# Optimization experiments

Measured on AMD Instinct MI355X. Metric: run time of the kernel, lower is better.

Reference implementation:

```python
import jax, jax.numpy as jnp
import numpy as np

AVG_NOBJ = 49.0
NEG_SLOPE = 0.01  # torch leaky_relu default


def eops_1_to_2(x, nobj, aggregation):
    """x: [B,N,C] -> [B,C,5,N,N] equivariant basis (rank-1 -> rank-2)."""
    B, N, C = x.shape
    xt = jnp.transpose(x, (0, 2, 1))  # B,C,N
    if aggregation == 'sum':
        agg = xt.sum(-1) / AVG_NOBJ                      # B,C
    elif aggregation == 'mean':
        agg = xt.sum(-1) / nobj[:, None]                 # B,C
    elif aggregation == 'max':
        agg = xt.max(-1)
    elif aggregation == 'min':
        agg = xt.min(-1)
    eye = jnp.eye(N, dtype=x.dtype)                      # N,N
    op1 = xt[:, :, :, None] * eye                        # x_i on diagonal
    op2 = jnp.broadcast_to(xt[:, :, None, :], (B, C, N, N))  # x_j along rows
    op3 = jnp.broadcast_to(xt[:, :, :, None], (B, C, N, N))  # x_i along cols
    op4 = agg[:, :, None, None] * eye                    # agg on diagonal
    op5 = jnp.broadcast_to(agg[:, :, None, None], (B, C, N, N))  # agg everywhere
    return jnp.stack([op1, op2, op3, op4, op5], axis=2)  # B,C,5,N,N


def setup_inputs() -> dict:
    key = jax.random.key(0)
    k1, k2 = jax.random.split(key)
    B, N, C, S = 8, 128, 64, 64
    basis_total = 5 * 4  # 5 basis ops per config char, config='smxn'
    inputs = jax.random.normal(k1, (B, N, C), dtype=jnp.float32)
    mask = jnp.ones((B, N, N, 1), dtype=jnp.float32)
    nobj = jnp.full((B,), 100.0, dtype=jnp.float32)
    coefs = jax.random.normal(k2, (C, S, basis_total), dtype=jnp.float32) * np.sqrt(2.0 / (C * basis_total)).astype(np.float32)
    bias = jnp.zeros((S,), dtype=jnp.float32)
    return {"inputs": inputs, "mask": mask, "nobj": nobj, "coefs": coefs, "bias": bias}


def reference(inputs, mask, nobj, coefs, bias):
    # config = 'smxn' -> sum, mean, max, min basis tensors, concat on basis axis
    ops = jnp.concatenate(
        [eops_1_to_2(inputs, nobj, a) for a in ('sum', 'mean', 'max', 'min')],
        axis=2)  # B,C,20,N,N
    out = jnp.einsum('dsb,ndbij->nijs', coefs, ops)      # B,N,N,S
    out = out + bias[None, None, None, :]
    out = jnp.where(out >= 0, out, NEG_SLOPE * out)      # leaky_relu
    return out * mask
```

## Files before the change

kernel.cpp:

```cpp
#include <hip/hip_runtime.h>

constexpr int B = 8, N = 128, C = 64, S = 64;
constexpr float INV_AVG = 1.0f / 49.0f;
constexpr float SLOPE = 0.01f;

typedef float f4 __attribute__((ext_vector_type(4)));

constexpr int WS_A  = 0;
constexpr int WS_R  = 65536;
constexpr int WS_C  = 131072;
constexpr int WS_D  = 196608;
constexpr int WS_E  = 197120;

__global__ __launch_bounds__(256) void prep_kernel(
    const float* __restrict__ x,
    const float* __restrict__ nobj,
    const float* __restrict__ coefs,
    float* __restrict__ ws)
{
  __shared__ float smem[13312];
  const int tid = threadIdx.x;

  if (blockIdx.x < 64) {
    float* W1 = smem;
    float* W2 = smem + 4096;
    float* W3 = smem + 8192;
    float* xs = smem + 12288;
    const int n  = blockIdx.x >> 3;
    const int i0 = (blockIdx.x & 7) << 4;

#pragma unroll
    for (int k = 0; k < 16; ++k) {
      const int e = k * 256 + tid;
      const float4* cp = (const float4*)(coefs + e * 20);
      float4 f0 = cp[0], f1 = cp[1], f2 = cp[2], f3 = cp[3], f4v = cp[4];
      W1[e] = f0.x + f1.y + f2.z + f3.w;
      W2[e] = f0.y + f1.z + f2.w + f4v.x;
      W3[e] = f0.z + f1.w + f3.x + f4v.y;
    }
    ((float4*)xs)[tid] = ((const float4*)(x + (n * N + i0) * C))[tid];
    __syncthreads();

    const int s = tid & 63;
    const int g = tid >> 6;
    float a1[4] = {0,0,0,0}, a2[4] = {0,0,0,0}, a3[4] = {0,0,0,0};
#pragma unroll 8
    for (int d = 0; d < 64; ++d) {
      float w1 = W1[d * 64 + s];
      float w2 = W2[d * 64 + s];
      float w3 = W3[d * 64 + s];
#pragma unroll
      for (int k = 0; k < 4; ++k) {
        float xv = xs[(g * 4 + k) * 64 + d];
        a1[k] += xv * w1;
        a2[k] += xv * w2;
        a3[k] += xv * w3;
      }
    }
#pragma unroll
    for (int k = 0; k < 4; ++k) {
      const int o = (n * N + i0 + g * 4 + k) * S + s;
      ws[WS_A + o] = a1[k];
      ws[WS_R + o] = a2[k];
      ws[WS_C + o] = a3[k];
    }
  } else {
    const int n = blockIdx.x - 64;
    float* xs  = smem;
    float* ps  = smem + 8192;
    float* pmx = smem + 8448;
    float* pmn = smem + 8704;
    float* ag  = smem + 8960;

    const float4* xg = (const float4*)(x + n * N * C);
    float4* xs4 = (float4*)xs;
#pragma unroll
    for (int k = 0; k < 8; ++k) xs4[tid + k * 256] = xg[tid + k * 256];
    __syncthreads();

    const int d = tid & 63, grp = tid >> 6;
    float sm = 0.f, mx = -INFINITY, mn = INFINITY;
    for (int i = grp * 32; i < grp * 32 + 32; ++i) {
      float v = xs[i * 64 + d];
      sm += v;
      mx = fmaxf(mx, v);
      mn = fminf(mn, v);
    }
    ps [grp * 64 + d] = sm;
    pmx[grp * 64 + d] = mx;
    pmn[grp * 64 + d] = mn;
    __syncthreads();

    if (tid < 64) {
      float s0 = ps[tid] + ps[64 + tid] + ps[128 + tid] + ps[192 + tid];
      float m0 = fmaxf(fmaxf(pmx[tid], pmx[64 + tid]),
                       fmaxf(pmx[128 + tid], pmx[192 + tid]));
      float n0 = fminf(fminf(pmn[tid], pmn[64 + tid]),
                       fminf(pmn[128 + tid], pmn[192 + tid]));
      ag[tid]       = s0 * INV_AVG;
      ag[64 + tid]  = s0 / nobj[n];
      ag[128 + tid] = m0;
      ag[192 + tid] = n0;
    }
    __syncthreads();

    if (tid < 64) {
      const int s = tid;
      float dv = 0.f, ev = 0.f;
      for (int d2 = 0; d2 < 64; ++d2) {
        const float* cp = coefs + d2 * (S * 20) + s * 20;
        float a0 = ag[d2], a1 = ag[64 + d2], a2 = ag[128 + d2], a3 = ag[192 + d2];
        dv += a0 * cp[3] + a1 * cp[8] + a2 * cp[13] + a3 * cp[18];
        ev += a0 * cp[4] + a1 * cp[9] + a2 * cp[14] + a3 * cp[19];
      }
      ws[WS_D + n * S + s] = dv;
      ws[WS_E + n * S + s] = ev;
    }
  }
}

__global__ __launch_bounds__(256) void assemble_kernel(
    const float* __restrict__ ws,
    const float* __restrict__ mask,
    const float* __restrict__ bias,
    float* __restrict__ out)
{
  const int bi = blockIdx.x;
  const int n  = bi >> 7;
  const int i  = bi & 127;
  const int l  = threadIdx.x & 15;
  const int jg = threadIdx.x >> 4;

  const float4* A4 = (const float4*)(ws + WS_A);
  const float4* R4 = (const float4*)(ws + WS_R);
  const float4* C4 = (const float4*)(ws + WS_C);
  const float4* D4 = (const float4*)(ws + WS_D);
  const float4* E4 = (const float4*)(ws + WS_E);

  float4 cc = C4[bi * 16 + l];
  float4 ee = E4[n * 16 + l];
  float4 bb = ((const float4*)bias)[l];
  float bx = cc.x + ee.x + bb.x;
  float by = cc.y + ee.y + bb.y;
  float bz = cc.z + ee.z + bb.z;
  float bw = cc.w + ee.w + bb.w;

  f4* out4 = (f4*)out + (size_t)bi * (N * 16);

#pragma unroll
  for (int t = 0; t < 8; ++t) {
    const int j = jg + t * 16;
    float4 rr = R4[(n * N + j) * 16 + l];
    float  m  = mask[bi * N + j];
    float v0 = bx + rr.x;
    float v1 = by + rr.y;
    float v2 = bz + rr.z;
    float v3 = bw + rr.w;
    if (j == i) {
      float4 aa = A4[bi * 16 + l];
      float4 dd = D4[n * 16 + l];
      v0 += aa.x + dd.x; v1 += aa.y + dd.y;
      v2 += aa.z + dd.z; v3 += aa.w + dd.w;
    }
    v0 = (v0 >= 0.f) ? v0 : SLOPE * v0;
    v1 = (v1 >= 0.f) ? v1 : SLOPE * v1;
    v2 = (v2 >= 0.f) ? v2 : SLOPE * v2;
    v3 = (v3 >= 0.f) ? v3 : SLOPE * v3;
    f4 o;
    o.x = v0 * m; o.y = v1 * m; o.z = v2 * m; o.w = v3 * m;
    __builtin_nontemporal_store(o, &out4[j * 16 + l]);
  }
}

extern "C" void kernel_launch(void* const* d_in, const int* in_sizes, int n_in,
                              void* d_out, int out_size, void* d_ws, size_t ws_size,
                              hipStream_t stream) {
  const float* x     = (const float*)d_in[0];
  const float* mask  = (const float*)d_in[1];
  const float* nobj  = (const float*)d_in[2];
  const float* coefs = (const float*)d_in[3];
  const float* bias  = (const float*)d_in[4];
  float* out = (float*)d_out;
  float* ws  = (float*)d_ws;

  prep_kernel<<<72, 256, 0, stream>>>(x, nobj, coefs, ws);
  assemble_kernel<<<1024, 256, 0, stream>>>(ws, mask, bias, out);
}
```

Baseline: 83.13 us.

## Fuse prep and assemble kernels into a single kernel with redundant per-block recompute

Merges the two-kernel pipeline into one kernel of 256 blocks. Each block handles 4 rows i and recomputes the per-batch aggregates, the combined coefficient matrices, the row term for all 128 j, and the D/E terms from shared memory, then writes the output directly. This removes the second launch and the workspace round trip through global memory. In exchange, every block redoes the 64x64 coefficient reduction and the R projection for its batch (32x redundant work), and there are fewer blocks to hide the store-bound output write.

```diff
diff --git a/kernel.cpp b/kernel.cpp
--- a/kernel.cpp
+++ b/kernel.cpp
@@ -1,174 +1,163 @@
 #include <hip/hip_runtime.h>
 
-constexpr int B = 8, N = 128, C = 64, S = 64;
+constexpr int N = 128, S = 64;
 constexpr float INV_AVG = 1.0f / 49.0f;
 constexpr float SLOPE = 0.01f;
 
 typedef float f4 __attribute__((ext_vector_type(4)));
 
-constexpr int WS_A  = 0;
-constexpr int WS_R  = 65536;
-constexpr int WS_C  = 131072;
-constexpr int WS_D  = 196608;
-constexpr int WS_E  = 197120;
-
-__global__ __launch_bounds__(256) void prep_kernel(
+__global__ __launch_bounds__(256) void fused_kernel(
     const float* __restrict__ x,
+    const float* __restrict__ mask,
     const float* __restrict__ nobj,
     const float* __restrict__ coefs,
-    float* __restrict__ ws)
+    const float* __restrict__ bias,
+    float* __restrict__ out)
 {
-  __shared__ float smem[13312];
+  __shared__ float xs[8192];
+  __shared__ float w2[4096];
+  __shared__ float ag[256];
+  __shared__ float part[2560];
+  __shared__ float fin[512];
+
   const int tid = threadIdx.x;
+  const int n   = blockIdx.x >> 5;
+  const int i0  = (blockIdx.x & 31) << 2;
 
-  if (blockIdx.x < 64) {
-    float* W1 = smem;
-    float* W2 = smem + 4096;
-    float* W3 = smem + 8192;
-    float* xs = smem + 12288;
-    const int n  = blockIdx.x >> 3;
-    const int i0 = (blockIdx.x & 7) << 4;
-
-#pragma unroll
-    for (int k = 0; k < 16; ++k) {
-      const int e = k * 256 + tid;
-      const float4* cp = (const float4*)(coefs + e * 20);
-      float4 f0 = cp[0], f1 = cp[1], f2 = cp[2], f3 = cp[3], f4v = cp[4];
-      W1[e] = f0.x + f1.y + f2.z + f3.w;
-      W2[e] = f0.y + f1.z + f2.w + f4v.x;
-      W3[e] = f0.z + f1.w + f3.x + f4v.y;
-    }
-    ((float4*)xs)[tid] = ((const float4*)(x + (n * N + i0) * C))[tid];
-    __syncthreads();
-
-    const int s = tid & 63;
-    const int g = tid >> 6;
-    float a1[4] = {0,0,0,0}, a2[4] = {0,0,0,0}, a3[4] = {0,0,0,0};
-#pragma unroll 8
-    for (int d = 0; d < 64; ++d) {
-      float w1 = W1[d * 64 + s];
-      float w2 = W2[d * 64 + s];
-      float w3 = W3[d * 64 + s];
-#pragma unroll
-      for (int k = 0; k < 4; ++k) {
-        float xv = xs[(g * 4 + k) * 64 + d];
-        a1[k] += xv * w1;
-        a2[k] += xv * w2;
-        a3[k] += xv * w3;
-      }
-    }
-#pragma unroll
-    for (int k = 0; k < 4; ++k) {
-      const int o = (n * N + i0 + g * 4 + k) * S + s;
-      ws[WS_A + o] = a1[k];
-      ws[WS_R + o] = a2[k];
-      ws[WS_C + o] = a3[k];
-    }
-  } else {
-    const int n = blockIdx.x - 64;
-    float* xs  = smem;
-    float* ps  = smem + 8192;
-    float* pmx = smem + 8448;
-    float* pmn = smem + 8704;
-    float* ag  = smem + 8960;
-
-    const float4* xg = (const float4*)(x + n * N * C);
+  {
+    const float4* xg = (const float4*)(x + n * N * 64);
     float4* xs4 = (float4*)xs;
 #pragma unroll
     for (int k = 0; k < 8; ++k) xs4[tid + k * 256] = xg[tid + k * 256];
-    __syncthreads();
+  }
+  __syncthreads();
 
+  {
     const int d = tid & 63, grp = tid >> 6;
     float sm = 0.f, mx = -INFINITY, mn = INFINITY;
     for (int i = grp * 32; i < grp * 32 + 32; ++i) {
       float v = xs[i * 64 + d];
-      sm += v;
-      mx = fmaxf(mx, v);
-      mn = fminf(mn, v);
+      sm += v; mx = fmaxf(mx, v); mn = fminf(mn, v);
     }
-    ps [grp * 64 + d] = sm;
-    pmx[grp * 64 + d] = mx;
-    pmn[grp * 64 + d] = mn;
-    __syncthreads();
+    part[grp * 64 + d]       = sm;
+    part[256 + grp * 64 + d] = mx;
+    part[512 + grp * 64 + d] = mn;
+  }
+  __syncthreads();
+  if (tid < 64) {
+    float s0 = part[tid] + part[64 + tid] + part[128 + tid] + part[192 + tid];
+    float m0 = fmaxf(fmaxf(part[256 + tid], part[320 + tid]),
+                     fmaxf(part[384 + tid], part[448 + tid]));
+    float n0 = fminf(fminf(part[512 + tid], part[576 + tid]),
+                     fminf(part[640 + tid], part[704 + tid]));
+    ag[tid]       = s0 * INV_AVG;
+    ag[64 + tid]  = s0 / nobj[n];
+    ag[128 + tid] = m0;
+    ag[192 + tid] = n0;
+  }
+  __syncthreads();
 
-    if (tid < 64) {
-      float s0 = ps[tid] + ps[64 + tid] + ps[128 + tid] + ps[192 + tid];
-      float m0 = fmaxf(fmaxf(pmx[tid], pmx[64 + tid]),
-                       fmaxf(pmx[128 + tid], pmx[192 + tid]));
-      float n0 = fminf(fminf(pmn[tid], pmn[64 + tid]),
-                       fminf(pmn[128 + tid], pmn[192 + tid]));
-      ag[tid]       = s0 * INV_AVG;
-      ag[64 + tid]  = s0 / nobj[n];
-      ag[128 + tid] = m0;
-      ag[192 + tid] = n0;
+  {
+    const int g = tid >> 6;
+    const int s = tid & 63;
+    float pA[4] = {0,0,0,0}, pC[4] = {0,0,0,0};
+    float pD = 0.f, pE = 0.f;
+#pragma unroll
+    for (int k = 0; k < 16; ++k) {
+      const int e = k * 256 + tid;
+      const int d = e >> 6;
+      const float4* cp = (const float4*)(coefs + e * 20);
+      float4 f0 = cp[0], f1 = cp[1], f2 = cp[2], f3 = cp[3], f4v = cp[4];
+      float w1v = f0.x + f1.y + f2.z + f3.w;
+      float w2v = f0.y + f1.z + f2.w + f4v.x;
+      float w3v = f0.z + f1.w + f3.x + f4v.y;
+      w2[e] = w2v;
+#pragma unroll
+      for (int m = 0; m < 4; ++m) {
+        float xv = xs[(i0 + m) * 64 + d];
+        pA[m] += xv * w1v;
+        pC[m] += xv * w3v;
+      }
+      pD += ag[d] * f0.w + ag[64 + d] * f2.x + ag[128 + d] * f3.y + ag[192 + d] * f4v.z;
+      pE += ag[d] * f1.x + ag[64 + d] * f2.y + ag[128 + d] * f3.z + ag[192 + d] * f4v.w;
     }
-    __syncthreads();
-
-    if (tid < 64) {
-      const int s = tid;
-      float dv = 0.f, ev = 0.f;
-      for (int d2 = 0; d2 < 64; ++d2) {
-        const float* cp = coefs + d2 * (S * 20) + s * 20;
-        float a0 = ag[d2], a1 = ag[64 + d2], a2 = ag[128 + d2], a3 = ag[192 + d2];
-        dv += a0 * cp[3] + a1 * cp[8] + a2 * cp[13] + a3 * cp[18];
-        ev += a0 * cp[4] + a1 * cp[9] + a2 * cp[14] + a3 * cp[19];
-      }
-      ws[WS_D + n * S + s] = dv;
-      ws[WS_E + n * S + s] = ev;
+#pragma unroll
+    for (int m = 0; m < 4; ++m) {
+      part[m * 256 + g * 64 + s]       = pA[m];
+      part[(4 + m) * 256 + g * 64 + s] = pC[m];
+    }
+    part[2048 + g * 64 + s] = pD;
+    part[2304 + g * 64 + s] = pE;
+  }
+  __syncthreads();
+  if (tid < 64) {
+    const int s = tid;
+    float D = part[2048 + s] + part[2048 + 64 + s] + part[2048 + 128 + s] + part[2048 + 192 + s];
+    float E = part[2304 + s] + part[2304 + 64 + s] + part[2304 + 128 + s] + part[2304 + 192 + s];
+    float bv = bias[s];
+#pragma unroll
+    for (int m = 0; m < 4; ++m) {
+      float A = part[m * 256 + s] + part[m * 256 + 64 + s]
+              + part[m * 256 + 128 + s] + part[m * 256 + 192 + s];
+      float C = part[(4 + m) * 256 + s] + part[(4 + m) * 256 + 64 + s]
+              + part[(4 + m) * 256 + 128 + s] + part[(4 + m) * 256 + 192 + s];
+      fin[m * 64 + s]       = C + E + bv;
+      fin[256 + m * 64 + s] = A + D;
     }
   }
-}
+  __syncthreads();
 
-__global__ __launch_bounds__(256) void assemble_kernel(
-    const float* __restrict__ ws,
-    const float* __restrict__ mask,
-    const float* __restrict__ bias,
-    float* __restrict__ out)
-{
-  const int bi = blockIdx.x;
-  const int n  = bi >> 7;
-  const int i  = bi & 127;
-  const int l  = threadIdx.x & 15;
-  const int jg = threadIdx.x >> 4;
+  const int l  = tid & 15;
+  const int jg = tid >> 4;
 
-  const float4* A4 = (const float4*)(ws + WS_A);
-  const float4* R4 = (const float4*)(ws + WS_R);
-  const float4* C4 = (const float4*)(ws + WS_C);
-  const float4* D4 = (const float4*)(ws + WS_D);
-  const float4* E4 = (const float4*)(ws + WS_E);
+  float4 base[4], diag[4];
+#pragma unroll
+  for (int m = 0; m < 4; ++m) {
+    base[m] = *(const float4*)&fin[m * 64 + l * 4];
+    diag[m] = *(const float4*)&fin[256 + m * 64 + l * 4];
+  }
 
-  float4 cc = C4[bi * 16 + l];
-  float4 ee = E4[n * 16 + l];
-  float4 bb = ((const float4*)bias)[l];
-  float bx = cc.x + ee.x + bb.x;
-  float by = cc.y + ee.y + bb.y;
-  float bz = cc.z + ee.z + bb.z;
-  float bw = cc.w + ee.w + bb.w;
+  float4 racc[8];
+#pragma unroll
+  for (int t = 0; t < 8; ++t) { racc[t].x = racc[t].y = racc[t].z = racc[t].w = 0.f; }
 
-  f4* out4 = (f4*)out + (size_t)bi * (N * 16);
+#pragma unroll 4
+  for (int d = 0; d < 64; ++d) {
+    float4 wq = *(const float4*)&w2[d * 64 + l * 4];
+#pragma unroll
+    for (int t = 0; t < 8; ++t) {
+      float xv = xs[(jg + 16 * t) * 64 + d];
+      racc[t].x += xv * wq.x;
+      racc[t].y += xv * wq.y;
+      racc[t].z += xv * wq.z;
+      racc[t].w += xv * wq.w;
+    }
+  }
 
+  f4* out4 = (f4*)out;
 #pragma unroll
   for (int t = 0; t < 8; ++t) {
-    const int j = jg + t * 16;
-    float4 rr = R4[(n * N + j) * 16 + l];
-    float  m  = mask[bi * N + j];
-    float v0 = bx + rr.x;
-    float v1 = by + rr.y;
-    float v2 = bz + rr.z;
-    float v3 = bw + rr.w;
-    if (j == i) {
-      float4 aa = A4[bi * 16 + l];
-      float4 dd = D4[n * 16 + l];
-      v0 += aa.x + dd.x; v1 += aa.y + dd.y;
-      v2 += aa.z + dd.z; v3 += aa.w + dd.w;
+    const int j = jg + 16 * t;
+#pragma unroll
+    for (int m = 0; m < 4; ++m) {
+      const int i = i0 + m;
+      float v0 = base[m].x + racc[t].x;
+      float v1 = base[m].y + racc[t].y;
+      float v2 = base[m].z + racc[t].z;
+      float v3 = base[m].w + racc[t].w;
+      if (j == i) {
+        v0 += diag[m].x; v1 += diag[m].y;
+        v2 += diag[m].z; v3 += diag[m].w;
+      }
+      v0 = (v0 >= 0.f) ? v0 : SLOPE * v0;
+      v1 = (v1 >= 0.f) ? v1 : SLOPE * v1;
+      v2 = (v2 >= 0.f) ? v2 : SLOPE * v2;
+      v3 = (v3 >= 0.f) ? v3 : SLOPE * v3;
+      float mk = mask[(n * N + i) * N + j];
+      f4 o;
+      o.x = v0 * mk; o.y = v1 * mk; o.z = v2 * mk; o.w = v3 * mk;
+      __builtin_nontemporal_store(o, &out4[(size_t)((n * N + i) * N + j) * 16 + l]);
     }
-    v0 = (v0 >= 0.f) ? v0 : SLOPE * v0;
-    v1 = (v1 >= 0.f) ? v1 : SLOPE * v1;
-    v2 = (v2 >= 0.f) ? v2 : SLOPE * v2;
-    v3 = (v3 >= 0.f) ? v3 : SLOPE * v3;
-    f4 o;
-    o.x = v0 * m; o.y = v1 * m; o.z = v2 * m; o.w = v3 * m;
-    __builtin_nontemporal_store(o, &out4[j * 16 + l]);
   }
 }
 
@@ -181,8 +170,6 @@
   const float* coefs = (const float*)d_in[3];
   const float* bias  = (const float*)d_in[4];
   float* out = (float*)d_out;
-  float* ws  = (float*)d_ws;
 
-  prep_kernel<<<72, 256, 0, stream>>>(x, nobj, coefs, ws);
-  assemble_kernel<<<1024, 256, 0, stream>>>(ws, mask, bias, out);
+  fused_kernel<<<256, 256, 0, stream>>>(x, mask, nobj, coefs, bias, out);
 }
```

Result: no change. 83.69 us (+0.7%).
